# Kernel optimization log

Hardware: AMD Instinct MI355X
Metric: run time of the kernel (lower is better)

## Reference

```python
import jax, jax.numpy as jnp
import numpy as np

N = 100000          # nodes
E = 1600000         # edges (nnz of A)
D_IN = 128
D_OUT = 128


def setup_inputs() -> dict:
    key = jax.random.key(0)
    ks = jax.random.split(key, 9)
    s = 1.0 / np.sqrt(D_IN)
    inp = {
        "h_n": jax.random.normal(ks[0], (N, D_IN), dtype=jnp.float32),
        "W_w": jax.random.uniform(ks[1], (D_OUT, D_IN), jnp.float32, -s, s),
        "W_b": jax.random.uniform(ks[2], (D_OUT,), jnp.float32, -s, s),
        "Wt_w": jax.random.uniform(ks[3], (D_OUT, D_IN), jnp.float32, -s, s),
        "Wt_b": jax.random.uniform(ks[4], (D_OUT,), jnp.float32, -s, s),
        "Ws_w": jax.random.uniform(ks[5], (D_OUT, D_IN), jnp.float32, -s, s),
        "Ws_b": jax.random.uniform(ks[6], (D_OUT,), jnp.float32, -s, s),
        # COO indices of sparse adjacency A (binary values): A[rows[e], cols[e]] = 1
        "rows": jax.random.randint(ks[7], (E,), 0, N, dtype=jnp.int64)
                if jax.config.jax_enable_x64 else
                jax.random.randint(ks[7], (E,), 0, N, dtype=jnp.int32),
        "cols": jax.random.randint(ks[8], (E,), 0, N, dtype=jnp.int32),
    }
    inp["rows"] = inp["rows"].astype(jnp.int32)
    return inp


def reference(h_n, W_w, W_b, Wt_w, Wt_b, Ws_w, Ws_b, rows, cols):
    # Dense projections: [N, D_OUT]
    Wh  = h_n @ W_w.T + W_b    # W(h_n)
    Wth = h_n @ Wt_w.T + Wt_b  # W_trans(h_n)
    Wsh = h_n @ Ws_w.T + Ws_b  # W_self(h_n)

    # A @ Wh  : out[i] = sum over edges (i=rows[e], j=cols[e]) of Wh[j]
    agg   = jax.ops.segment_sum(Wh[cols],  rows, num_segments=N)
    # A_T @ Wth : out[i] = sum over edges (j=rows[e], i=cols[e]) of Wth[j]
    agg_t = jax.ops.segment_sum(Wth[rows], cols, num_segments=N)

    # exact (erf-based) GELU, matching torch F.gelu default
    return jax.nn.gelu(agg + agg_t + Wsh, approximate=False)
```

## Files before the change

### kernel.cpp

```cpp
#include <hip/hip_runtime.h>


typedef __bf16 bf16;
typedef __bf16 bf16x4 __attribute__((ext_vector_type(4)));
typedef __bf16 bf16x8 __attribute__((ext_vector_type(8)));
typedef float  f32x4  __attribute__((ext_vector_type(4)));
typedef unsigned int u32;
typedef u32 u32x4 __attribute__((ext_vector_type(4)));
typedef unsigned short u16;

#define D 128
#define CAPC 2432
#define SLAB 2816
#define BIN_CHUNK 12544

__global__ void k_cast(const float* __restrict__ h,
                       const float* __restrict__ Ws_w, const float* __restrict__ W_w,
                       const float* __restrict__ Wt_w,
                       bf16* __restrict__ h_bf, bf16* __restrict__ wbf, int n4h) {
    int i = blockIdx.x * 256 + threadIdx.x;
    if (i < n4h) {
        f32x4 v = *(const f32x4*)&h[i * 4];
        bf16x4 o;
        o.x = (bf16)v.x; o.y = (bf16)v.y; o.z = (bf16)v.z; o.w = (bf16)v.w;
        *(bf16x4*)&h_bf[i * 4] = o;
    } else if (i < n4h + 32) {
        int k = i - n4h;
        bf16x4 z; z.x = (bf16)0.f; z.y = (bf16)0.f; z.z = (bf16)0.f; z.w = (bf16)0.f;
        *(bf16x4*)&h_bf[(size_t)n4h * 4 + k * 4] = z;
    } else {
        int k = i - n4h - 32;
        if (k < 12288) {
            const float* src = (k < 4096) ? Ws_w : (k < 8192) ? W_w : Wt_w;
            int kk = k & 4095;
            f32x4 v = *(const f32x4*)&src[kk * 4];
            bf16x4 o;
            o.x = (bf16)v.x; o.y = (bf16)v.y; o.z = (bf16)v.z; o.w = (bf16)v.w;
            *(bf16x4*)&wbf[k * 4] = o;
        }
    }
}

__global__ __launch_bounds__(256) void k_bin(
    const int* __restrict__ rows, const int* __restrict__ cols,
    int* __restrict__ gcnt_f, int* __restrict__ gcnt_r,
    u32* __restrict__ buf_f, u32* __restrict__ buf_r, int E, int B) {
    __shared__ int hist[1024];
    __shared__ int lbase[1024];
    __shared__ int gbase[1024];
    __shared__ int tsum[256];
    __shared__ u32 sorted[BIN_CHUNK];
    __shared__ u16 btag[BIN_CHUNK];
    int t = threadIdx.x;
    int dir = blockIdx.y;
    const int* key = dir ? cols : rows;
    const int* pay = dir ? rows : cols;
    int* gcnt = dir ? gcnt_r : gcnt_f;
    u32* buf  = dir ? buf_r : buf_f;
    int base = blockIdx.x * BIN_CHUNK;

    for (int b = t; b < 1024; b += 256) hist[b] = 0;
    __syncthreads();
    for (int i = 0; i < BIN_CHUNK / 256; ++i) {
        int e = base + i * 256 + t;
        if (e < E) atomicAdd(&hist[key[e] >> 7], 1);
    }
    __syncthreads();
    int s0 = hist[t * 4], s1 = hist[t * 4 + 1], s2 = hist[t * 4 + 2], s3 = hist[t * 4 + 3];
    tsum[t] = s0 + s1 + s2 + s3;
    __syncthreads();
    for (int o = 1; o < 256; o <<= 1) {
        int v = (t >= o) ? tsum[t - o] : 0;
        __syncthreads();
        tsum[t] += v;
        __syncthreads();
    }
    int run = (t > 0) ? tsum[t - 1] : 0;
    lbase[t * 4]     = run;
    lbase[t * 4 + 1] = run + s0;
    lbase[t * 4 + 2] = run + s0 + s1;
    lbase[t * 4 + 3] = run + s0 + s1 + s2;
    __syncthreads();
    int total = tsum[255];
    for (int b = t; b < 1024; b += 256) {
        int nxt = (b < 1023) ? lbase[b + 1] : total;
        int c = nxt - lbase[b];
        gbase[b] = (c && b < B) ? atomicAdd(&gcnt[b], c) : 0;
        hist[b] = lbase[b];
    }
    __syncthreads();
    for (int i = 0; i < BIN_CHUNK / 256; ++i) {
        int e = base + i * 256 + t;
        if (e < E) {
            int k = key[e], p = pay[e];
            int b = k >> 7;
            int pos = atomicAdd(&hist[b], 1);
            sorted[pos] = ((u32)(k & 127) << 17) | (u32)p;
            btag[pos] = (u16)b;
        }
    }
    __syncthreads();
    for (int i = t; i < total; i += 256) {
        int b = btag[i];
        int gp = gbase[b] + (i - lbase[b]);
        if (gp < CAPC) buf[(size_t)b * SLAB + gp] = sorted[i];
    }
}

__global__ __launch_bounds__(256) void k_sort(
    const int* __restrict__ cnt_f, const int* __restrict__ cnt_r,
    u32* __restrict__ buf_f, u32* __restrict__ buf_r,
    int* __restrict__ off_f, int* __restrict__ off_r,
    int* __restrict__ deg_f, int* __restrict__ deg_r, int N, u32 PADV) {
    __shared__ u32 words[CAPC];
    __shared__ u32 sorted[SLAB];
    __shared__ int hist[128], pscn[128], cur[128];
    int t = threadIdx.x, bkt = blockIdx.x;
    const int* cp; u32* buf; int* off; int* deg;
    if (blockIdx.y == 0) { cp = cnt_f; buf = buf_f + (size_t)bkt * SLAB; off = off_f; deg = deg_f; }
    else                 { cp = cnt_r; buf = buf_r + (size_t)bkt * SLAB; off = off_r; deg = deg_r; }
    int cnt = cp[bkt]; if (cnt > CAPC) cnt = CAPC;
    if (t < 128) hist[t] = 0;
    __syncthreads();
    for (int i = t; i < cnt; i += 256) {
        u32 w = buf[i]; words[i] = w;
        atomicAdd(&hist[w >> 17], 1);
    }
    __syncthreads();
    int pd = 0;
    if (t < 128) { pd = (hist[t] + 3) & ~3; pscn[t] = pd; }
    __syncthreads();
    for (int o = 1; o < 128; o <<= 1) {
        int v = (t < 128 && t >= o) ? pscn[t - o] : 0;
        __syncthreads();
        if (t < 128) pscn[t] += v;
        __syncthreads();
    }
    int ptot = pscn[127];
    int node0 = bkt * 128;
    if (t < 128) {
        int pstart = pscn[t] - pd;
        cur[t] = pstart;
        int node = node0 + t;
        if (node < N) { off[node] = bkt * SLAB + pstart; deg[node] = hist[t]; }
    }
    __syncthreads();
    for (int i = t; i < ptot; i += 256) sorted[i] = PADV;
    __syncthreads();
    for (int i = t; i < cnt; i += 256) {
        u32 w = words[i];
        int p = atomicAdd(&cur[w >> 17], 1);
        sorted[p] = (w & 0x1FFFF) << 6;
    }
    __syncthreads();
    for (int i = t; i < ptot; i += 256) buf[i] = sorted[i];
}

__device__ __forceinline__ float blo(u32 w) { return __uint_as_float(w << 16); }
__device__ __forceinline__ float bhi(u32 w) { return __uint_as_float(w & 0xffff0000u); }

__global__ void k_agg(const u32* __restrict__ h32,
                      const int* __restrict__ off_f, const int* __restrict__ deg_f,
                      const u32* __restrict__ buf_f,
                      const int* __restrict__ off_r, const int* __restrict__ deg_r,
                      const u32* __restrict__ buf_r,
                      bf16* __restrict__ AH, bf16* __restrict__ ATH, int N) {
    int wave = threadIdx.x >> 6, lane = threadIdx.x & 63;
    int node = blockIdx.x * 4 + wave;
    if (node >= N) return;
    const int* off; const int* deg; const u32* idx; bf16* dst;
    if (blockIdx.y == 0) { off = off_f; deg = deg_f; idx = buf_f; dst = AH; }
    else                 { off = off_r; deg = deg_r; idx = buf_r; dst = ATH; }
    int p = off[node];
    int pend = p + ((deg[node] + 3) & ~3);
    int q = lane >> 4, c = lane & 15;
    float a0 = 0.f, a1 = 0.f, a2 = 0.f, a3 = 0.f;
    float a4 = 0.f, a5 = 0.f, a6 = 0.f, a7 = 0.f;
    for (; p + 15 < pend; p += 16) {
        u32 j0 = idx[p + q], j1 = idx[p + 4 + q];
        u32 j2 = idx[p + 8 + q], j3 = idx[p + 12 + q];
        u32x4 w0 = *(const u32x4*)&h32[(size_t)j0 + c * 4];
        u32x4 w1 = *(const u32x4*)&h32[(size_t)j1 + c * 4];
        u32x4 w2 = *(const u32x4*)&h32[(size_t)j2 + c * 4];
        u32x4 w3 = *(const u32x4*)&h32[(size_t)j3 + c * 4];
        a0 += blo(w0.x); a1 += bhi(w0.x); a2 += blo(w0.y); a3 += bhi(w0.y);
        a4 += blo(w0.z); a5 += bhi(w0.z); a6 += blo(w0.w); a7 += bhi(w0.w);
        a0 += blo(w1.x); a1 += bhi(w1.x); a2 += blo(w1.y); a3 += bhi(w1.y);
        a4 += blo(w1.z); a5 += bhi(w1.z); a6 += blo(w1.w); a7 += bhi(w1.w);
        a0 += blo(w2.x); a1 += bhi(w2.x); a2 += blo(w2.y); a3 += bhi(w2.y);
        a4 += blo(w2.z); a5 += bhi(w2.z); a6 += blo(w2.w); a7 += bhi(w2.w);
        a0 += blo(w3.x); a1 += bhi(w3.x); a2 += blo(w3.y); a3 += bhi(w3.y);
        a4 += blo(w3.z); a5 += bhi(w3.z); a6 += blo(w3.w); a7 += bhi(w3.w);
    }
    for (; p + 3 < pend; p += 4) {
        u32 j = idx[p + q];
        u32x4 w = *(const u32x4*)&h32[(size_t)j + c * 4];
        a0 += blo(w.x); a1 += bhi(w.x); a2 += blo(w.y); a3 += bhi(w.y);
        a4 += blo(w.z); a5 += bhi(w.z); a6 += blo(w.w); a7 += bhi(w.w);
    }
    a0 += __shfl_down(a0, 16); a1 += __shfl_down(a1, 16);
    a2 += __shfl_down(a2, 16); a3 += __shfl_down(a3, 16);
    a4 += __shfl_down(a4, 16); a5 += __shfl_down(a5, 16);
    a6 += __shfl_down(a6, 16); a7 += __shfl_down(a7, 16);
    a0 += __shfl_down(a0, 32); a1 += __shfl_down(a1, 32);
    a2 += __shfl_down(a2, 32); a3 += __shfl_down(a3, 32);
    a4 += __shfl_down(a4, 32); a5 += __shfl_down(a5, 32);
    a6 += __shfl_down(a6, 32); a7 += __shfl_down(a7, 32);
    if (lane < 16) {
        bf16x8 o;
        o[0] = (bf16)a0; o[1] = (bf16)a1; o[2] = (bf16)a2; o[3] = (bf16)a3;
        o[4] = (bf16)a4; o[5] = (bf16)a5; o[6] = (bf16)a6; o[7] = (bf16)a7;
        *(bf16x8*)&dst[(size_t)node * D + c * 8] = o;
    }
}

__global__ __launch_bounds__(256) void k_gemm(
    const bf16* __restrict__ h, const bf16* __restrict__ AH, const bf16* __restrict__ ATH,
    const bf16* __restrict__ wbf,
    const float* __restrict__ Ws_b, const float* __restrict__ W_b, const float* __restrict__ Wt_b,
    const int* __restrict__ deg_out, const int* __restrict__ deg_in,
    float* __restrict__ out, int N) {
    __shared__ __align__(16) bf16 Ash[128 * 32];
    __shared__ __align__(16) bf16 Bsh[128 * 32];
    int t = threadIdx.x;
    int lane = t & 63;
    int w = t >> 6;
    int wm = (w >> 1) * 64, wn = (w & 1) * 64;
    int m0 = blockIdx.x * 128;

    f32x4 acc[4][4];
#pragma unroll
    for (int i = 0; i < 4; ++i)
#pragma unroll
        for (int j = 0; j < 4; ++j)
            acc[i][j] = (f32x4){0.f, 0.f, 0.f, 0.f};

    for (int kc = 0; kc < 12; ++kc) {
        const bf16* X  = (kc < 4) ? h : (kc < 8) ? AH : ATH;
        const bf16* Wm = wbf + (kc >> 2) * (128 * 128);
        int c0 = (kc & 3) * 32;
#pragma unroll
        for (int r = 0; r < 2; ++r) {
            int v = r * 256 + t;
            int row = v >> 2, seg = v & 3;
            int xr = m0 + row; if (xr >= N) xr = N - 1;
            *(bf16x8*)&Ash[row * 32 + seg * 8] =
                *(const bf16x8*)&X[(size_t)xr * D + c0 + seg * 8];
            *(bf16x8*)&Bsh[row * 32 + seg * 8] =
                *(const bf16x8*)&Wm[row * D + c0 + seg * 8];
        }
        __syncthreads();
        int kg = lane >> 4, lr = lane & 15;
        bf16x8 a[4], b[4];
#pragma unroll
        for (int i = 0; i < 4; ++i) {
            a[i] = *(const bf16x8*)&Ash[(wm + i * 16 + lr) * 32 + kg * 8];
            b[i] = *(const bf16x8*)&Bsh[(wn + i * 16 + lr) * 32 + kg * 8];
        }
#pragma unroll
        for (int i = 0; i < 4; ++i)
#pragma unroll
            for (int j = 0; j < 4; ++j)
                acc[i][j] = __builtin_amdgcn_mfma_f32_16x16x32_bf16(
                    a[i], b[j], acc[i][j], 0, 0, 0);
        __syncthreads();
    }

    int lr = lane & 15, lq = lane >> 4;
#pragma unroll
    for (int i = 0; i < 4; ++i) {
#pragma unroll
        for (int r = 0; r < 4; ++r) {
            int node = m0 + wm + i * 16 + lq * 4 + r;
            if (node >= N) continue;
            float fdr = (float)deg_out[node], fdc = (float)deg_in[node];
#pragma unroll
            for (int j = 0; j < 4; ++j) {
                int f = wn + j * 16 + lr;
                float val = acc[i][j][r] + Ws_b[f] + fdr * W_b[f] + fdc * Wt_b[f];
                float g = 0.5f * val * (1.0f + erff(val * 0.70710678118654752f));
                out[(size_t)node * D + f] = g;
            }
        }
    }
}

extern "C" void kernel_launch(void* const* d_in, const int* in_sizes, int n_in,
                              void* d_out, int out_size, void* d_ws, size_t ws_size,
                              hipStream_t stream) {
    const float* h    = (const float*)d_in[0];
    const float* W_w  = (const float*)d_in[1];
    const float* W_b  = (const float*)d_in[2];
    const float* Wt_w = (const float*)d_in[3];
    const float* Wt_b = (const float*)d_in[4];
    const float* Ws_w = (const float*)d_in[5];
    const float* Ws_b = (const float*)d_in[6];
    const int*   rows = (const int*)d_in[7];
    const int*   cols = (const int*)d_in[8];
    float* out = (float*)d_out;

    const int N = in_sizes[0] / D;
    const int E = in_sizes[7];
    const int B = (N + 127) >> 7;

    char* ws = (char*)d_ws;
    size_t off = 0;
    auto take = [&](size_t bytes) -> char* {
        char* p = ws + off;
        off += (bytes + 511) & ~(size_t)511;
        return p;
    };
    bf16* h_bf    = (bf16*)take((size_t)(N + 1) * D * sizeof(bf16));
    bf16* AH      = (bf16*)take((size_t)N * D * sizeof(bf16));
    bf16* ATH     = (bf16*)take((size_t)N * D * sizeof(bf16));
    bf16* wbf     = (bf16*)take((size_t)3 * 128 * 128 * sizeof(bf16));
    int*  gcnt    = (int*)take((size_t)2 * B * sizeof(int));
    int*  off_f   = (int*)take((size_t)N * sizeof(int));
    int*  off_r   = (int*)take((size_t)N * sizeof(int));
    int*  deg_f   = (int*)take((size_t)N * sizeof(int));
    int*  deg_r   = (int*)take((size_t)N * sizeof(int));
    u32*  buf_f   = (u32*)take((size_t)B * SLAB * sizeof(u32));
    u32*  buf_r   = (u32*)take((size_t)B * SLAB * sizeof(u32));
    int*  gcnt_f = gcnt, *gcnt_r = gcnt + B;

    hipMemsetAsync(gcnt, 0, (size_t)2 * B * sizeof(int), stream);

    int n4h = N * D / 4;
    int ncast = n4h + 32 + 3 * 128 * 128 / 4;
    k_cast<<<(ncast + 255) / 256, 256, 0, stream>>>(h, Ws_w, W_w, Wt_w,
                                                    h_bf, wbf, n4h);

    dim3 gbin((E + BIN_CHUNK - 1) / BIN_CHUNK, 2);
    k_bin<<<gbin, 256, 0, stream>>>(rows, cols, gcnt_f, gcnt_r, buf_f, buf_r, E, B);
    dim3 gsort(B, 2);
    k_sort<<<gsort, 256, 0, stream>>>(gcnt_f, gcnt_r, buf_f, buf_r,
                                      off_f, off_r, deg_f, deg_r, N, (u32)N << 6);
    dim3 gagg((N + 3) / 4, 2);
    k_agg<<<gagg, 256, 0, stream>>>((const u32*)h_bf, off_f, deg_f, buf_f,
                                    off_r, deg_r, buf_r, AH, ATH, N);
    k_gemm<<<B, 256, 0, stream>>>(h_bf, AH, ATH, wbf,
                                  Ws_b, W_b, Wt_b,
                                  deg_f, deg_r, out, N);
}
```

Measured before the change: 329.7 us.

## Fuse bucket sort into aggregation and fold cast into binning kernel

The cast of h and the weights to bf16 now runs as a third grid slice of the binning kernel, and the binning chunk size is halved. The per-bucket sort and the neighbor aggregation are merged so that each block sorts its 128-node bucket in shared memory and gathers directly from the LDS-sorted indices. This removes two launches, the offset arrays and the write-back and re-read of sorted indices through global memory. In exchange, aggregation parallelism drops from one wave per node across a large grid to only about 2*782 blocks of 4 waves, which risks poor latency hiding on the gather. The larger shared-memory footprint of the fused kernel may also limit occupancy.

Result: faster. 317.8 us (-3.6%).

```diff
diff --git a/kernel.cpp b/kernel.cpp
--- a/kernel.cpp
+++ b/kernel.cpp
@@ -12,39 +12,16 @@
 #define D 128
 #define CAPC 2432
 #define SLAB 2816
-#define BIN_CHUNK 12544
-
-__global__ void k_cast(const float* __restrict__ h,
-                       const float* __restrict__ Ws_w, const float* __restrict__ W_w,
-                       const float* __restrict__ Wt_w,
-                       bf16* __restrict__ h_bf, bf16* __restrict__ wbf, int n4h) {
-    int i = blockIdx.x * 256 + threadIdx.x;
-    if (i < n4h) {
-        f32x4 v = *(const f32x4*)&h[i * 4];
-        bf16x4 o;
-        o.x = (bf16)v.x; o.y = (bf16)v.y; o.z = (bf16)v.z; o.w = (bf16)v.w;
-        *(bf16x4*)&h_bf[i * 4] = o;
-    } else if (i < n4h + 32) {
-        int k = i - n4h;
-        bf16x4 z; z.x = (bf16)0.f; z.y = (bf16)0.f; z.z = (bf16)0.f; z.w = (bf16)0.f;
-        *(bf16x4*)&h_bf[(size_t)n4h * 4 + k * 4] = z;
-    } else {
-        int k = i - n4h - 32;
-        if (k < 12288) {
-            const float* src = (k < 4096) ? Ws_w : (k < 8192) ? W_w : Wt_w;
-            int kk = k & 4095;
-            f32x4 v = *(const f32x4*)&src[kk * 4];
-            bf16x4 o;
-            o.x = (bf16)v.x; o.y = (bf16)v.y; o.z = (bf16)v.z; o.w = (bf16)v.w;
-            *(bf16x4*)&wbf[k * 4] = o;
-        }
-    }
-}
+#define BIN_CHUNK 6400
 
 __global__ __launch_bounds__(256) void k_bin(
     const int* __restrict__ rows, const int* __restrict__ cols,
     int* __restrict__ gcnt_f, int* __restrict__ gcnt_r,
-    u32* __restrict__ buf_f, u32* __restrict__ buf_r, int E, int B) {
+    u32* __restrict__ buf_f, u32* __restrict__ buf_r, int E, int B,
+    const float* __restrict__ h,
+    const float* __restrict__ Ws_w, const float* __restrict__ W_w,
+    const float* __restrict__ Wt_w,
+    bf16* __restrict__ h_bf, bf16* __restrict__ wbf, int n4h) {
     __shared__ int hist[1024];
     __shared__ int lbase[1024];
     __shared__ int gbase[1024];
@@ -52,6 +29,33 @@
     __shared__ u32 sorted[BIN_CHUNK];
     __shared__ u16 btag[BIN_CHUNK];
     int t = threadIdx.x;
+
+    if (blockIdx.y == 2) {
+        int stride = gridDim.x * 256;
+        int ncast = n4h + 32 + 12288;
+        for (int i = blockIdx.x * 256 + t; i < ncast; i += stride) {
+            if (i < n4h) {
+                f32x4 v = *(const f32x4*)&h[i * 4];
+                bf16x4 o;
+                o.x = (bf16)v.x; o.y = (bf16)v.y; o.z = (bf16)v.z; o.w = (bf16)v.w;
+                *(bf16x4*)&h_bf[i * 4] = o;
+            } else if (i < n4h + 32) {
+                int k = i - n4h;
+                bf16x4 z; z.x = (bf16)0.f; z.y = (bf16)0.f; z.z = (bf16)0.f; z.w = (bf16)0.f;
+                *(bf16x4*)&h_bf[(size_t)n4h * 4 + k * 4] = z;
+            } else {
+                int k = i - n4h - 32;
+                const float* src = (k < 4096) ? Ws_w : (k < 8192) ? W_w : Wt_w;
+                int kk = k & 4095;
+                f32x4 v = *(const f32x4*)&src[kk * 4];
+                bf16x4 o;
+                o.x = (bf16)v.x; o.y = (bf16)v.y; o.z = (bf16)v.z; o.w = (bf16)v.w;
+                *(bf16x4*)&wbf[k * 4] = o;
+            }
+        }
+        return;
+    }
+
     int dir = blockIdx.y;
     const int* key = dir ? cols : rows;
     const int* pay = dir ? rows : cols;
@@ -107,18 +111,22 @@
     }
 }
 
-__global__ __launch_bounds__(256) void k_sort(
-    const int* __restrict__ cnt_f, const int* __restrict__ cnt_r,
-    u32* __restrict__ buf_f, u32* __restrict__ buf_r,
-    int* __restrict__ off_f, int* __restrict__ off_r,
+__device__ __forceinline__ float blo(u32 w) { return __uint_as_float(w << 16); }
+__device__ __forceinline__ float bhi(u32 w) { return __uint_as_float(w & 0xffff0000u); }
+
+__global__ __launch_bounds__(256) void k_aggsort(
+    const u32* __restrict__ h32,
+    const int* __restrict__ gcnt_f, const int* __restrict__ gcnt_r,
+    const u32* __restrict__ buf_f, const u32* __restrict__ buf_r,
+    bf16* __restrict__ AH, bf16* __restrict__ ATH,
     int* __restrict__ deg_f, int* __restrict__ deg_r, int N, u32 PADV) {
     __shared__ u32 words[CAPC];
     __shared__ u32 sorted[SLAB];
-    __shared__ int hist[128], pscn[128], cur[128];
+    __shared__ int hist[128], pscn[128], cursor[128];
     int t = threadIdx.x, bkt = blockIdx.x;
-    const int* cp; u32* buf; int* off; int* deg;
-    if (blockIdx.y == 0) { cp = cnt_f; buf = buf_f + (size_t)bkt * SLAB; off = off_f; deg = deg_f; }
-    else                 { cp = cnt_r; buf = buf_r + (size_t)bkt * SLAB; off = off_r; deg = deg_r; }
+    const int* cp; const u32* buf; bf16* dst; int* deg;
+    if (blockIdx.y == 0) { cp = gcnt_f; buf = buf_f + (size_t)bkt * SLAB; dst = AH;  deg = deg_f; }
+    else                 { cp = gcnt_r; buf = buf_r + (size_t)bkt * SLAB; dst = ATH; deg = deg_r; }
     int cnt = cp[bkt]; if (cnt > CAPC) cnt = CAPC;
     if (t < 128) hist[t] = 0;
     __syncthreads();
@@ -137,80 +145,68 @@
         __syncthreads();
     }
     int ptot = pscn[127];
-    int node0 = bkt * 128;
-    if (t < 128) {
-        int pstart = pscn[t] - pd;
-        cur[t] = pstart;
-        int node = node0 + t;
-        if (node < N) { off[node] = bkt * SLAB + pstart; deg[node] = hist[t]; }
-    }
+    if (t < 128) cursor[t] = pscn[t] - pd;
     __syncthreads();
     for (int i = t; i < ptot; i += 256) sorted[i] = PADV;
     __syncthreads();
     for (int i = t; i < cnt; i += 256) {
         u32 w = words[i];
-        int p = atomicAdd(&cur[w >> 17], 1);
+        int p = atomicAdd(&cursor[w >> 17], 1);
         sorted[p] = (w & 0x1FFFF) << 6;
     }
     __syncthreads();
-    for (int i = t; i < ptot; i += 256) buf[i] = sorted[i];
-}
-
-__device__ __forceinline__ float blo(u32 w) { return __uint_as_float(w << 16); }
-__device__ __forceinline__ float bhi(u32 w) { return __uint_as_float(w & 0xffff0000u); }
-
-__global__ void k_agg(const u32* __restrict__ h32,
-                      const int* __restrict__ off_f, const int* __restrict__ deg_f,
-                      const u32* __restrict__ buf_f,
-                      const int* __restrict__ off_r, const int* __restrict__ deg_r,
-                      const u32* __restrict__ buf_r,
-                      bf16* __restrict__ AH, bf16* __restrict__ ATH, int N) {
-    int wave = threadIdx.x >> 6, lane = threadIdx.x & 63;
-    int node = blockIdx.x * 4 + wave;
-    if (node >= N) return;
-    const int* off; const int* deg; const u32* idx; bf16* dst;
-    if (blockIdx.y == 0) { off = off_f; deg = deg_f; idx = buf_f; dst = AH; }
-    else                 { off = off_r; deg = deg_r; idx = buf_r; dst = ATH; }
-    int p = off[node];
-    int pend = p + ((deg[node] + 3) & ~3);
+
+    int wave = t >> 6, lane = t & 63;
     int q = lane >> 4, c = lane & 15;
-    float a0 = 0.f, a1 = 0.f, a2 = 0.f, a3 = 0.f;
-    float a4 = 0.f, a5 = 0.f, a6 = 0.f, a7 = 0.f;
-    for (; p + 15 < pend; p += 16) {
-        u32 j0 = idx[p + q], j1 = idx[p + 4 + q];
-        u32 j2 = idx[p + 8 + q], j3 = idx[p + 12 + q];
-        u32x4 w0 = *(const u32x4*)&h32[(size_t)j0 + c * 4];
-        u32x4 w1 = *(const u32x4*)&h32[(size_t)j1 + c * 4];
-        u32x4 w2 = *(const u32x4*)&h32[(size_t)j2 + c * 4];
-        u32x4 w3 = *(const u32x4*)&h32[(size_t)j3 + c * 4];
-        a0 += blo(w0.x); a1 += bhi(w0.x); a2 += blo(w0.y); a3 += bhi(w0.y);
-        a4 += blo(w0.z); a5 += bhi(w0.z); a6 += blo(w0.w); a7 += bhi(w0.w);
-        a0 += blo(w1.x); a1 += bhi(w1.x); a2 += blo(w1.y); a3 += bhi(w1.y);
-        a4 += blo(w1.z); a5 += bhi(w1.z); a6 += blo(w1.w); a7 += bhi(w1.w);
-        a0 += blo(w2.x); a1 += bhi(w2.x); a2 += blo(w2.y); a3 += bhi(w2.y);
-        a4 += blo(w2.z); a5 += bhi(w2.z); a6 += blo(w2.w); a7 += bhi(w2.w);
-        a0 += blo(w3.x); a1 += bhi(w3.x); a2 += blo(w3.y); a3 += bhi(w3.y);
-        a4 += blo(w3.z); a5 += bhi(w3.z); a6 += blo(w3.w); a7 += bhi(w3.w);
-    }
-    for (; p + 3 < pend; p += 4) {
-        u32 j = idx[p + q];
-        u32x4 w = *(const u32x4*)&h32[(size_t)j + c * 4];
-        a0 += blo(w.x); a1 += bhi(w.x); a2 += blo(w.y); a3 += bhi(w.y);
-        a4 += blo(w.z); a5 += bhi(w.z); a6 += blo(w.w); a7 += bhi(w.w);
-    }
-    a0 += __shfl_down(a0, 16); a1 += __shfl_down(a1, 16);
-    a2 += __shfl_down(a2, 16); a3 += __shfl_down(a3, 16);
-    a4 += __shfl_down(a4, 16); a5 += __shfl_down(a5, 16);
-    a6 += __shfl_down(a6, 16); a7 += __shfl_down(a7, 16);
-    a0 += __shfl_down(a0, 32); a1 += __shfl_down(a1, 32);
-    a2 += __shfl_down(a2, 32); a3 += __shfl_down(a3, 32);
-    a4 += __shfl_down(a4, 32); a5 += __shfl_down(a5, 32);
-    a6 += __shfl_down(a6, 32); a7 += __shfl_down(a7, 32);
-    if (lane < 16) {
-        bf16x8 o;
-        o[0] = (bf16)a0; o[1] = (bf16)a1; o[2] = (bf16)a2; o[3] = (bf16)a3;
-        o[4] = (bf16)a4; o[5] = (bf16)a5; o[6] = (bf16)a6; o[7] = (bf16)a7;
-        *(bf16x8*)&dst[(size_t)node * D + c * 8] = o;
+    int node0 = bkt * 128;
+    for (int ln = wave; ln < 128; ln += 4) {
+        int node = node0 + ln;
+        if (node >= N) continue;
+        int dg = hist[ln];
+        int plen = (dg + 3) & ~3;
+        int p = pscn[ln] - plen, pend = pscn[ln];
+        float a0 = 0.f, a1 = 0.f, a2 = 0.f, a3 = 0.f;
+        float a4 = 0.f, a5 = 0.f, a6 = 0.f, a7 = 0.f;
+        for (; p + 15 < pend; p += 16) {
+            u32 j0 = sorted[p + q],     j1 = sorted[p + 4 + q];
+            u32 j2 = sorted[p + 8 + q], j3 = sorted[p + 12 + q];
+            u32x4 w0 = *(const u32x4*)&h32[(size_t)j0 + c * 4];
+            u32x4 w1 = *(const u32x4*)&h32[(size_t)j1 + c * 4];
+            u32x4 w2 = *(const u32x4*)&h32[(size_t)j2 + c * 4];
+            u32x4 w3 = *(const u32x4*)&h32[(size_t)j3 + c * 4];
+            a0 += blo(w0.x); a1 += bhi(w0.x); a2 += blo(w0.y); a3 += bhi(w0.y);
+            a4 += blo(w0.z); a5 += bhi(w0.z); a6 += blo(w0.w); a7 += bhi(w0.w);
+            a0 += blo(w1.x); a1 += bhi(w1.x); a2 += blo(w1.y); a3 += bhi(w1.y);
+            a4 += blo(w1.z); a5 += bhi(w1.z); a6 += blo(w1.w); a7 += bhi(w1.w);
+            a0 += blo(w2.x); a1 += bhi(w2.x); a2 += blo(w2.y); a3 += bhi(w2.y);
+            a4 += blo(w2.z); a5 += bhi(w2.z); a6 += blo(w2.w); a7 += bhi(w2.w);
+            a0 += blo(w3.x); a1 += bhi(w3.x); a2 += blo(w3.y); a3 += bhi(w3.y);
+            a4 += blo(w3.z); a5 += bhi(w3.z); a6 += blo(w3.w); a7 += bhi(w3.w);
+        }
+        for (; p + 3 < pend; p += 4) {
+            u32 j = sorted[p + q];
+            u32x4 w = *(const u32x4*)&h32[(size_t)j + c * 4];
+            a0 += blo(w.x); a1 += bhi(w.x); a2 += blo(w.y); a3 += bhi(w.y);
+            a4 += blo(w.z); a5 += bhi(w.z); a6 += blo(w.w); a7 += bhi(w.w);
+        }
+        a0 += __shfl_down(a0, 16); a1 += __shfl_down(a1, 16);
+        a2 += __shfl_down(a2, 16); a3 += __shfl_down(a3, 16);
+        a4 += __shfl_down(a4, 16); a5 += __shfl_down(a5, 16);
+        a6 += __shfl_down(a6, 16); a7 += __shfl_down(a7, 16);
+        a0 += __shfl_down(a0, 32); a1 += __shfl_down(a1, 32);
+        a2 += __shfl_down(a2, 32); a3 += __shfl_down(a3, 32);
+        a4 += __shfl_down(a4, 32); a5 += __shfl_down(a5, 32);
+        a6 += __shfl_down(a6, 32); a7 += __shfl_down(a7, 32);
+        if (lane < 16) {
+            bf16x8 o;
+            o[0] = (bf16)a0; o[1] = (bf16)a1; o[2] = (bf16)a2; o[3] = (bf16)a3;
+            o[4] = (bf16)a4; o[5] = (bf16)a5; o[6] = (bf16)a6; o[7] = (bf16)a7;
+            *(bf16x8*)&dst[(size_t)node * D + c * 8] = o;
+        }
+    }
+    if (t < 128) {
+        int node = node0 + t;
+        if (node < N) deg[node] = hist[t];
     }
 }
 
@@ -315,8 +311,6 @@
     bf16* ATH     = (bf16*)take((size_t)N * D * sizeof(bf16));
     bf16* wbf     = (bf16*)take((size_t)3 * 128 * 128 * sizeof(bf16));
     int*  gcnt    = (int*)take((size_t)2 * B * sizeof(int));
-    int*  off_f   = (int*)take((size_t)N * sizeof(int));
-    int*  off_r   = (int*)take((size_t)N * sizeof(int));
     int*  deg_f   = (int*)take((size_t)N * sizeof(int));
     int*  deg_r   = (int*)take((size_t)N * sizeof(int));
     u32*  buf_f   = (u32*)take((size_t)B * SLAB * sizeof(u32));
@@ -326,18 +320,13 @@
     hipMemsetAsync(gcnt, 0, (size_t)2 * B * sizeof(int), stream);
 
     int n4h = N * D / 4;
-    int ncast = n4h + 32 + 3 * 128 * 128 / 4;
-    k_cast<<<(ncast + 255) / 256, 256, 0, stream>>>(h, Ws_w, W_w, Wt_w,
-                                                    h_bf, wbf, n4h);
-
-    dim3 gbin((E + BIN_CHUNK - 1) / BIN_CHUNK, 2);
-    k_bin<<<gbin, 256, 0, stream>>>(rows, cols, gcnt_f, gcnt_r, buf_f, buf_r, E, B);
-    dim3 gsort(B, 2);
-    k_sort<<<gsort, 256, 0, stream>>>(gcnt_f, gcnt_r, buf_f, buf_r,
-                                      off_f, off_r, deg_f, deg_r, N, (u32)N << 6);
-    dim3 gagg((N + 3) / 4, 2);
-    k_agg<<<gagg, 256, 0, stream>>>((const u32*)h_bf, off_f, deg_f, buf_f,
-                                    off_r, deg_r, buf_r, AH, ATH, N);
+    dim3 gbin((E + BIN_CHUNK - 1) / BIN_CHUNK, 3);
+    k_bin<<<gbin, 256, 0, stream>>>(rows, cols, gcnt_f, gcnt_r, buf_f, buf_r,
+                                    E, B, h, Ws_w, W_w, Wt_w, h_bf, wbf, n4h);
+    dim3 gagg(B, 2);
+    k_aggsort<<<gagg, 256, 0, stream>>>((const u32*)h_bf, gcnt_f, gcnt_r,
+                                        buf_f, buf_r, AH, ATH,
+                                        deg_f, deg_r, N, (u32)N << 6);
     k_gemm<<<B, 256, 0, stream>>>(h_bf, AH, ATH, wbf,
                                   Ws_b, W_b, Wt_b,
                                   deg_f, deg_r, out, N);
```
